# Kernel tuning notes

Hardware: AMD Instinct MI355X
Metric: run time of the kernel (lower is better)

Reference implementation:

```python
import jax, jax.numpy as jnp
import numpy as np

B, S, D, H = 2, 2048, 1024, 16
HD = D // H


def setup_inputs() -> dict:
    key = jax.random.key(0)
    ks = jax.random.split(key, 9)
    std = 0.02
    return {
        "x": jax.random.normal(ks[0], (B, S, D), dtype=jnp.float32),
        "wq": jax.random.normal(ks[1], (D, D), dtype=jnp.float32) * std,
        "bq": jnp.zeros((D,), dtype=jnp.float32),
        "wk": jax.random.normal(ks[2], (D, D), dtype=jnp.float32) * std,
        "bk": jnp.zeros((D,), dtype=jnp.float32),
        "wv": jax.random.normal(ks[3], (D, D), dtype=jnp.float32) * std,
        "bv": jnp.zeros((D,), dtype=jnp.float32),
        "wo": jax.random.normal(ks[4], (D, D), dtype=jnp.float32) * std,
        "bo": jnp.zeros((D,), dtype=jnp.float32),
    }


def reference(x, wq, bq, wk, bk, wv, bv, wo, bo):
    bsz, seq_len, d_model = x.shape
    # projections: torch Linear computes x @ W.T + b with W of shape (out, in)
    q = (x @ wq.T + bq).reshape(bsz, seq_len, H, HD).transpose(0, 2, 1, 3)  # bhsd
    k = (x @ wk.T + bk).reshape(bsz, seq_len, H, HD).transpose(0, 2, 1, 3)
    v = (x @ wv.T + bv).reshape(bsz, seq_len, H, HD).transpose(0, 2, 1, 3)
    scale = HD ** -0.5
    scores = jnp.einsum("bhqd,bhkd->bhqk", q, k) * scale  # [B,H,S,S]
    causal = jnp.tril(jnp.ones((seq_len, seq_len), dtype=bool))
    scores = jnp.where(causal[None, None], scores, -jnp.inf)
    attn = jax.nn.softmax(scores, axis=-1)
    ctx = jnp.einsum("bhqk,bhkd->bhqd", attn, v)
    ctx = ctx.transpose(0, 2, 1, 3).reshape(bsz, seq_len, d_model)
    return ctx @ wo.T + bo
```

## Files before the change

### kernel.cpp

```cpp
#include <hip/hip_runtime.h>
#include <hip/hip_bf16.h>

#define B_  2
#define S_  2048
#define D_  1024
#define H_  16
#define HD_ 64
#define M_  (B_ * S_)

typedef __bf16 bf16;
typedef __bf16 bf16x4 __attribute__((ext_vector_type(4)));
typedef __bf16 bf16x8 __attribute__((ext_vector_type(8)));
typedef float  f32x4  __attribute__((ext_vector_type(4)));

__device__ __forceinline__ bf16x8 ld8g(const bf16* p) { return *(const bf16x8*)p; }

#define GLL(g, l) __builtin_amdgcn_global_load_lds( \
    (const __attribute__((address_space(1))) void*)(g), \
    (__attribute__((address_space(3))) void*)(l), 16, 0, 0)

__global__ __launch_bounds__(256) void convert_kernel(
    const float* __restrict__ x,  const float* __restrict__ wq,
    const float* __restrict__ wk, const float* __restrict__ wv,
    const float* __restrict__ wo,
    bf16* __restrict__ xb,  bf16* __restrict__ wqb, bf16* __restrict__ wkb,
    bf16* __restrict__ wvb, bf16* __restrict__ wob)
{
    const int seg = blockIdx.y;
    const float* src;
    bf16* dst;
    if (seg < 4)      { src = x  + (long)seg * 1048576; dst = xb  + (long)seg * 1048576; }
    else if (seg == 4){ src = wq; dst = wqb; }
    else if (seg == 5){ src = wk; dst = wkb; }
    else if (seg == 6){ src = wv; dst = wvb; }
    else              { src = wo; dst = wob; }
    const long i = ((long)blockIdx.x * 256 + threadIdx.x) * 8;
    float4 a = *(const float4*)(src + i);
    float4 b = *(const float4*)(src + i + 4);
    bf16x8 r;
    r[0] = (bf16)a.x; r[1] = (bf16)a.y; r[2] = (bf16)a.z; r[3] = (bf16)a.w;
    r[4] = (bf16)b.x; r[5] = (bf16)b.y; r[6] = (bf16)b.z; r[7] = (bf16)b.w;
    *(bf16x8*)(dst + i) = r;
}

__device__ __forceinline__ void gemm_acc_bk32(
    const bf16* __restrict__ A, const bf16* __restrict__ Bt,
    f32x4 (&acc)[4][4])
{
    __shared__ bf16 As[128 * 32];
    __shared__ bf16 Bs[128 * 32];

    const int tid  = threadIdx.x;
    const int wave = tid >> 6;
    const int lane = tid & 63;
    const int quad = lane >> 4;
    const int l15  = lane & 15;
    const int wr   = (wave >> 1) * 64;
    const int wc   = (wave & 1) * 64;
    const int m0   = blockIdx.y * 128;
    const int n0   = blockIdx.x * 128;

    const int sr = wave * 16 + (lane >> 2);
    const int sc = (lane & 3) * 8;
    const bf16* Ag = A  + (long)(m0 + sr) * D_ + sc;
    const bf16* Bg = Bt + (long)(n0 + sr) * D_ + sc;
    bf16* lA = As + wave * 512;
    bf16* lB = Bs + wave * 512;

    for (int k0 = 0; k0 < D_; k0 += 32) {
        __syncthreads();
        GLL(Ag + k0,             lA);
        GLL(Ag + 64 * D_ + k0,   lA + 64 * 32);
        GLL(Bg + k0,             lB);
        GLL(Bg + 64 * D_ + k0,   lB + 64 * 32);
        __syncthreads();

        bf16x8 af[4], bfr[4];
        for (int mi = 0; mi < 4; mi++)
            af[mi] = *(const bf16x8*)&As[(wr + mi * 16 + l15) * 32 + quad * 8];
        for (int ni = 0; ni < 4; ni++)
            bfr[ni] = *(const bf16x8*)&Bs[(wc + ni * 16 + l15) * 32 + quad * 8];

        for (int mi = 0; mi < 4; mi++)
            for (int ni = 0; ni < 4; ni++)
                acc[mi][ni] = __builtin_amdgcn_mfma_f32_16x16x32_bf16(
                    af[mi], bfr[ni], acc[mi][ni], 0, 0, 0);
    }
}

__global__ __launch_bounds__(256) void gemm_qkv(
    const bf16* __restrict__ xb,
    const bf16* __restrict__ wqb, const bf16* __restrict__ wkb, const bf16* __restrict__ wvb,
    const float* __restrict__ bq, const float* __restrict__ bk, const float* __restrict__ bv,
    bf16* __restrict__ qb, bf16* __restrict__ kb, bf16* __restrict__ vt)
{
    const bf16*  Bt   = (blockIdx.z == 0) ? wqb : (blockIdx.z == 1) ? wkb : wvb;
    const float* bias = (blockIdx.z == 0) ? bq  : (blockIdx.z == 1) ? bk  : bv;

    f32x4 acc[4][4] = {};
    gemm_acc_bk32(xb, Bt, acc);

    const int lane = threadIdx.x & 63;
    const int wave = threadIdx.x >> 6;
    const int quad = lane >> 4;
    const int l15  = lane & 15;
    const int wr   = (wave >> 1) * 64;
    const int wc   = (wave & 1) * 64;
    const int m0   = blockIdx.y * 128;
    const int n0   = blockIdx.x * 128;

    if (blockIdx.z < 2) {
        bf16* Cout = (blockIdx.z == 0) ? qb : kb;
        for (int ni = 0; ni < 4; ni++) {
            const int col = n0 + wc + ni * 16 + l15;
            const float bv = bias[col];
            for (int mi = 0; mi < 4; mi++) {
                const int rowb = m0 + wr + mi * 16 + quad * 4;
                for (int r = 0; r < 4; r++)
                    Cout[(long)(rowb + r) * D_ + col] = (bf16)(acc[mi][ni][r] + bv);
            }
        }
    } else {
        for (int ni = 0; ni < 4; ni++) {
            const int col = n0 + wc + ni * 16 + l15;
            const float bv = bias[col];
            const int h = col >> 6, hd = col & (HD_ - 1);
            for (int mi = 0; mi < 4; mi++) {
                const int rowb = m0 + wr + mi * 16 + quad * 4;
                const int b = rowb >> 11;
                const int s0 = rowb & (S_ - 1);
                bf16x4 v4;
                for (int r = 0; r < 4; r++) v4[r] = (bf16)(acc[mi][ni][r] + bv);
                *(bf16x4*)&vt[(((long)(b * H_ + h)) * HD_ + hd) * S_ + s0] = v4;
            }
        }
    }
}

__global__ __launch_bounds__(256) void gemm_out(
    const bf16* __restrict__ cb, const bf16* __restrict__ wob,
    const float* __restrict__ bo, float* __restrict__ out)
{
    f32x4 acc[4][4] = {};
    gemm_acc_bk32(cb, wob, acc);

    const int lane = threadIdx.x & 63;
    const int wave = threadIdx.x >> 6;
    const int quad = lane >> 4;
    const int l15  = lane & 15;
    const int wr   = (wave >> 1) * 64;
    const int wc   = (wave & 1) * 64;
    const int m0   = blockIdx.y * 128;
    const int n0   = blockIdx.x * 128;

    for (int ni = 0; ni < 4; ni++) {
        const int col = n0 + wc + ni * 16 + l15;
        const float bv = bo[col];
        for (int mi = 0; mi < 4; mi++) {
            const int rowb = m0 + wr + mi * 16 + quad * 4;
            for (int r = 0; r < 4; r++)
                out[(long)(rowb + r) * D_ + col] = acc[mi][ni][r] + bv;
        }
    }
}

__global__ __launch_bounds__(512) void attn_kernel(
    const bf16* __restrict__ Q, const bf16* __restrict__ K,
    const bf16* __restrict__ vt, bf16* __restrict__ ctx)
{
    constexpr int LDK = 72;
    __shared__ bf16 Ks[2][64 * LDK];
    __shared__ bf16 Vt[2][64 * LDK];
    __shared__ bf16 Pq[8][16 * LDK];

    const int tid  = threadIdx.x;
    const int wave = tid >> 6;
    const int lane = tid & 63;
    const int quad = lane >> 4;
    const int l15  = lane & 15;
    const int bh   = blockIdx.y;
    const int qt   = (blockIdx.y < 16) ? blockIdx.x : (15 - (int)blockIdx.x);
    const int b    = bh >> 4, h = bh & 15;
    const long base  = ((long)b * S_) * D_ + h * HD_;
    const bf16* Vth  = vt + (long)bh * HD_ * S_;

    const int krow = tid >> 3;
    const int kcol = (tid & 7) * 8;

    const int qw    = qt * 128 + wave * 16;
    const int qrow  = qw + l15;
    const bf16* Qr = Q + base + (long)qrow * D_;
    bf16x8 qf0 = ld8g(&Qr[quad * 8]);
    bf16x8 qf1 = ld8g(&Qr[quad * 8 + 32]);

    float l_i = 0.f;
    f32x4 o_acc[4] = {};

    auto process_tile = [&](int kbase, int buf) {
        if (kbase > qw + 15) return;
        f32x4 sc[4];
        for (int kt = 0; kt < 4; kt++) {
            const bf16* Kr = &Ks[buf][(kt * 16 + l15) * LDK + quad * 8];
            bf16x8 a0 = *(const bf16x8*)Kr;
            bf16x8 a1 = *(const bf16x8*)(Kr + 32);
            f32x4 z = {};
            z = __builtin_amdgcn_mfma_f32_16x16x32_bf16(a0, qf0, z, 0, 0, 0);
            z = __builtin_amdgcn_mfma_f32_16x16x32_bf16(a1, qf1, z, 0, 0, 0);
            sc[kt] = z;
        }
        float sum = 0.f;
        if (kbase + 63 > qw) {
            for (int kt = 0; kt < 4; kt++)
                for (int r = 0; r < 4; r++) {
                    const int k_g = kbase + kt * 16 + quad * 4 + r;
                    const float p = (k_g <= qrow) ? __expf(sc[kt][r] * 0.125f) : 0.f;
                    sc[kt][r] = p;
                    sum += p;
                }
        } else {
            for (int kt = 0; kt < 4; kt++)
                for (int r = 0; r < 4; r++) {
                    const float p = __expf(sc[kt][r] * 0.125f);
                    sc[kt][r] = p;
                    sum += p;
                }
        }
        sum += __shfl_xor(sum, 16, 64);
        sum += __shfl_xor(sum, 32, 64);
        l_i += sum;

        bf16* Pw = &Pq[wave][0];
        for (int kt = 0; kt < 4; kt++) {
            union { uint2 u; bf16 hh[4]; } pk;
            pk.hh[0] = (bf16)sc[kt][0];
            pk.hh[1] = (bf16)sc[kt][1];
            pk.hh[2] = (bf16)sc[kt][2];
            pk.hh[3] = (bf16)sc[kt][3];
            *(uint2*)&Pw[l15 * LDK + kt * 16 + quad * 4] = pk.u;
        }
        __asm__ volatile("s_waitcnt lgkmcnt(0)" ::: "memory");
        bf16x8 pf0 = *(const bf16x8*)&Pw[l15 * LDK + quad * 8];
        bf16x8 pf1 = *(const bf16x8*)&Pw[l15 * LDK + quad * 8 + 32];

        for (int ni = 0; ni < 4; ni++) {
            const bf16* Vr = &Vt[buf][(ni * 16 + l15) * LDK + quad * 8];
            bf16x8 av0 = *(const bf16x8*)Vr;
            bf16x8 av1 = *(const bf16x8*)(Vr + 32);
            o_acc[ni] = __builtin_amdgcn_mfma_f32_16x16x32_bf16(av0, pf0, o_acc[ni], 0, 0, 0);
            o_acc[ni] = __builtin_amdgcn_mfma_f32_16x16x32_bf16(av1, pf1, o_acc[ni], 0, 0, 0);
        }
    };

    bf16x8 kA = ld8g(K + base + (long)krow * D_ + kcol);
    bf16x8 wA = ld8g(Vth + (long)krow * S_ + kcol);
    bf16x8 kB = ld8g(K + base + (long)(64 + krow) * D_ + kcol);
    bf16x8 wB = ld8g(Vth + (long)krow * S_ + 64 + kcol);

    const int njt = 2 * qt + 2;
    for (int j = 0; j < njt; j += 2) {
        __syncthreads();
        *(bf16x8*)&Ks[0][krow * LDK + kcol] = kA;
        *(bf16x8*)&Vt[0][krow * LDK + kcol] = wA;
        *(bf16x8*)&Ks[1][krow * LDK + kcol] = kB;
        *(bf16x8*)&Vt[1][krow * LDK + kcol] = wB;
        if (j + 2 < njt) {
            kA = ld8g(K + base + (long)((j + 2) * 64 + krow) * D_ + kcol);
            wA = ld8g(Vth + (long)krow * S_ + (j + 2) * 64 + kcol);
            kB = ld8g(K + base + (long)((j + 3) * 64 + krow) * D_ + kcol);
            wB = ld8g(Vth + (long)krow * S_ + (j + 3) * 64 + kcol);
        }
        __syncthreads();
        process_tile(j * 64, 0);
        process_tile(j * 64 + 64, 1);
    }

    const float invl = 1.f / l_i;
    bf16* Pw = &Pq[wave][0];
    for (int ni = 0; ni < 4; ni++)
        for (int r = 0; r < 4; r++)
            Pw[l15 * LDK + ni * 16 + quad * 4 + r] = (bf16)(o_acc[ni][r] * invl);
    __asm__ volatile("s_waitcnt lgkmcnt(0)" ::: "memory");
    for (int round = 0; round < 2; round++) {
        const int rowq = (lane >> 3) + round * 8;
        bf16x8 val = *(const bf16x8*)&Pw[rowq * LDK + (lane & 7) * 8];
        const int q_g = qt * 128 + wave * 16 + rowq;
        *(bf16x8*)&ctx[base + (long)q_g * D_ + (lane & 7) * 8] = val;
    }
}

extern "C" void kernel_launch(void* const* d_in, const int* in_sizes, int n_in,
                              void* d_out, int out_size, void* d_ws, size_t ws_size,
                              hipStream_t stream)
{
    const float* x  = (const float*)d_in[0];
    const float* wq = (const float*)d_in[1];
    const float* bq = (const float*)d_in[2];
    const float* wk = (const float*)d_in[3];
    const float* bk = (const float*)d_in[4];
    const float* wv = (const float*)d_in[5];
    const float* bv = (const float*)d_in[6];
    const float* wo = (const float*)d_in[7];
    const float* bo = (const float*)d_in[8];
    float* out = (float*)d_out;

    const long NX = (long)M_ * D_;
    const long NW = (long)D_ * D_;
    bf16* xb  = (bf16*)d_ws;
    bf16* wqb = xb  + NX;
    bf16* wkb = wqb + NW;
    bf16* wvb = wkb + NW;
    bf16* wob = wvb + NW;
    bf16* qb  = wob + NW;
    bf16* kb  = qb  + NX;
    bf16* vt  = kb  + NX;
    bf16* cb  = xb;

    dim3 blk(256, 1, 1);

    convert_kernel<<<dim3(512, 8), blk, 0, stream>>>(
        x, wq, wk, wv, wo, xb, wqb, wkb, wvb, wob);

    gemm_qkv<<<dim3(8, 32, 3), blk, 0, stream>>>(
        xb, wqb, wkb, wvb, bq, bk, bv, qb, kb, vt);

    attn_kernel<<<dim3(16, 32), dim3(512, 1, 1), 0, stream>>>(qb, kb, vt, cb);

    gemm_out<<<dim3(8, 32), blk, 0, stream>>>(cb, wob, bo, out);
}
```

Measured before the change: 182.7 us.

## Remap block indices for XCD locality and shrink output GEMM tiles

```diff
diff --git a/kernel.cpp b/kernel.cpp
--- a/kernel.cpp
+++ b/kernel.cpp
@@ -45,7 +45,7 @@
 
 __device__ __forceinline__ void gemm_acc_bk32(
     const bf16* __restrict__ A, const bf16* __restrict__ Bt,
-    f32x4 (&acc)[4][4])
+    f32x4 (&acc)[4][4], int m0, int n0)
 {
     __shared__ bf16 As[128 * 32];
     __shared__ bf16 Bs[128 * 32];
@@ -57,8 +57,6 @@
     const int l15  = lane & 15;
     const int wr   = (wave >> 1) * 64;
     const int wc   = (wave & 1) * 64;
-    const int m0   = blockIdx.y * 128;
-    const int n0   = blockIdx.x * 128;
 
     const int sr = wave * 16 + (lane >> 2);
     const int sc = (lane & 3) * 8;
@@ -94,11 +92,18 @@
     const float* __restrict__ bq, const float* __restrict__ bk, const float* __restrict__ bv,
     bf16* __restrict__ qb, bf16* __restrict__ kb, bf16* __restrict__ vt)
 {
-    const bf16*  Bt   = (blockIdx.z == 0) ? wqb : (blockIdx.z == 1) ? wkb : wvb;
-    const float* bias = (blockIdx.z == 0) ? bq  : (blockIdx.z == 1) ? bk  : bv;
+    const int bid = blockIdx.x;
+    const int z   = bid >> 8;
+    const int r   = bid & 255;
+    const int Y   = (r & 7) * 4 + ((r >> 3) & 3);
+    const int X   = r >> 5;
+    const int m0  = Y * 128, n0 = X * 128;
+
+    const bf16*  Bt   = (z == 0) ? wqb : (z == 1) ? wkb : wvb;
+    const float* bias = (z == 0) ? bq  : (z == 1) ? bk  : bv;
 
     f32x4 acc[4][4] = {};
-    gemm_acc_bk32(xb, Bt, acc);
+    gemm_acc_bk32(xb, Bt, acc, m0, n0);
 
     const int lane = threadIdx.x & 63;
     const int wave = threadIdx.x >> 6;
@@ -106,18 +111,16 @@
     const int l15  = lane & 15;
     const int wr   = (wave >> 1) * 64;
     const int wc   = (wave & 1) * 64;
-    const int m0   = blockIdx.y * 128;
-    const int n0   = blockIdx.x * 128;
-
-    if (blockIdx.z < 2) {
-        bf16* Cout = (blockIdx.z == 0) ? qb : kb;
+
+    if (z < 2) {
+        bf16* Cout = (z == 0) ? qb : kb;
         for (int ni = 0; ni < 4; ni++) {
             const int col = n0 + wc + ni * 16 + l15;
             const float bv = bias[col];
             for (int mi = 0; mi < 4; mi++) {
                 const int rowb = m0 + wr + mi * 16 + quad * 4;
-                for (int r = 0; r < 4; r++)
-                    Cout[(long)(rowb + r) * D_ + col] = (bf16)(acc[mi][ni][r] + bv);
+                for (int r2 = 0; r2 < 4; r2++)
+                    Cout[(long)(rowb + r2) * D_ + col] = (bf16)(acc[mi][ni][r2] + bv);
             }
         }
     } else {
@@ -130,7 +133,7 @@
                 const int b = rowb >> 11;
                 const int s0 = rowb & (S_ - 1);
                 bf16x4 v4;
-                for (int r = 0; r < 4; r++) v4[r] = (bf16)(acc[mi][ni][r] + bv);
+                for (int r2 = 0; r2 < 4; r2++) v4[r2] = (bf16)(acc[mi][ni][r2] + bv);
                 *(bf16x4*)&vt[(((long)(b * H_ + h)) * HD_ + hd) * S_ + s0] = v4;
             }
         }
@@ -141,45 +144,78 @@
     const bf16* __restrict__ cb, const bf16* __restrict__ wob,
     const float* __restrict__ bo, float* __restrict__ out)
 {
-    f32x4 acc[4][4] = {};
-    gemm_acc_bk32(cb, wob, acc);
-
-    const int lane = threadIdx.x & 63;
-    const int wave = threadIdx.x >> 6;
-    const int quad = lane >> 4;
-    const int l15  = lane & 15;
-    const int wr   = (wave >> 1) * 64;
-    const int wc   = (wave & 1) * 64;
-    const int m0   = blockIdx.y * 128;
-    const int n0   = blockIdx.x * 128;
-
-    for (int ni = 0; ni < 4; ni++) {
-        const int col = n0 + wc + ni * 16 + l15;
-        const float bv = bo[col];
-        for (int mi = 0; mi < 4; mi++) {
-            const int rowb = m0 + wr + mi * 16 + quad * 4;
-            for (int r = 0; r < 4; r++)
-                out[(long)(rowb + r) * D_ + col] = acc[mi][ni][r] + bv;
-        }
-    }
-}
-
-__global__ __launch_bounds__(512) void attn_kernel(
-    const bf16* __restrict__ Q, const bf16* __restrict__ K,
-    const bf16* __restrict__ vt, bf16* __restrict__ ctx)
-{
-    constexpr int LDK = 72;
-    __shared__ bf16 Ks[2][64 * LDK];
-    __shared__ bf16 Vt[2][64 * LDK];
-    __shared__ bf16 Pq[8][16 * LDK];
+    __shared__ bf16 As[128 * 32];
+    __shared__ bf16 Bs[64 * 32];
+
+    const int bid = blockIdx.x;
+    const int Y   = (bid & 7) * 4 + ((bid >> 3) & 3);
+    const int X   = bid >> 5;
+    const int m0  = Y * 128, n0 = X * 64;
 
     const int tid  = threadIdx.x;
     const int wave = tid >> 6;
     const int lane = tid & 63;
     const int quad = lane >> 4;
     const int l15  = lane & 15;
-    const int bh   = blockIdx.y;
-    const int qt   = (blockIdx.y < 16) ? blockIdx.x : (15 - (int)blockIdx.x);
+    const int wr   = (wave >> 1) * 64;
+    const int wc   = (wave & 1) * 32;
+
+    const int sr = wave * 16 + (lane >> 2);
+    const int sc = (lane & 3) * 8;
+    const bf16* Ag = cb  + (long)(m0 + sr) * D_ + sc;
+    const bf16* Bg = wob + (long)(n0 + sr) * D_ + sc;
+    bf16* lA = As + wave * 512;
+    bf16* lB = Bs + wave * 512;
+
+    f32x4 acc[4][2] = {};
+
+    for (int k0 = 0; k0 < D_; k0 += 32) {
+        __syncthreads();
+        GLL(Ag + k0,             lA);
+        GLL(Ag + 64 * D_ + k0,   lA + 64 * 32);
+        GLL(Bg + k0,             lB);
+        __syncthreads();
+
+        bf16x8 af[4], bfr[2];
+        for (int mi = 0; mi < 4; mi++)
+            af[mi] = *(const bf16x8*)&As[(wr + mi * 16 + l15) * 32 + quad * 8];
+        for (int ni = 0; ni < 2; ni++)
+            bfr[ni] = *(const bf16x8*)&Bs[(wc + ni * 16 + l15) * 32 + quad * 8];
+
+        for (int mi = 0; mi < 4; mi++)
+            for (int ni = 0; ni < 2; ni++)
+                acc[mi][ni] = __builtin_amdgcn_mfma_f32_16x16x32_bf16(
+                    af[mi], bfr[ni], acc[mi][ni], 0, 0, 0);
+    }
+
+    for (int ni = 0; ni < 2; ni++) {
+        const int col = n0 + wc + ni * 16 + l15;
+        const float bv = bo[col];
+        for (int mi = 0; mi < 4; mi++) {
+            const int rowb = m0 + wr + mi * 16 + quad * 4;
+            for (int r2 = 0; r2 < 4; r2++)
+                out[(long)(rowb + r2) * D_ + col] = acc[mi][ni][r2] + bv;
+        }
+    }
+}
+
+__global__ __launch_bounds__(512) void attn_kernel(
+    const bf16* __restrict__ Q, const bf16* __restrict__ K,
+    const bf16* __restrict__ vt, bf16* __restrict__ ctx)
+{
+    constexpr int LDK = 72;
+    __shared__ bf16 Ks[2][64 * LDK];
+    __shared__ bf16 Vt[2][64 * LDK];
+    __shared__ bf16 Pq[8][16 * LDK];
+
+    const int tid  = threadIdx.x;
+    const int wave = tid >> 6;
+    const int lane = tid & 63;
+    const int quad = lane >> 4;
+    const int l15  = lane & 15;
+    const int bh   = blockIdx.x;
+    const int qy   = blockIdx.y;
+    const int qt   = (qy < 8) ? qy : (23 - qy);
     const int b    = bh >> 4, h = bh & 15;
     const long base  = ((long)b * S_) * D_ + h * HD_;
     const bf16* Vth  = vt + (long)bh * HD_ * S_;
@@ -320,10 +356,10 @@
     convert_kernel<<<dim3(512, 8), blk, 0, stream>>>(
         x, wq, wk, wv, wo, xb, wqb, wkb, wvb, wob);
 
-    gemm_qkv<<<dim3(8, 32, 3), blk, 0, stream>>>(
+    gemm_qkv<<<dim3(768, 1, 1), blk, 0, stream>>>(
         xb, wqb, wkb, wvb, bq, bk, bv, qb, kb, vt);
 
-    attn_kernel<<<dim3(16, 32), dim3(512, 1, 1), 0, stream>>>(qb, kb, vt, cb);
-
-    gemm_out<<<dim3(8, 32), blk, 0, stream>>>(cb, wob, bo, out);
-}
+    attn_kernel<<<dim3(32, 16), dim3(512, 1, 1), 0, stream>>>(qb, kb, vt, cb);
+
+    gemm_out<<<dim3(512, 1, 1), blk, 0, stream>>>(cb, wob, bo, out);
+}
```

Result: slower. 187.5 us (+2.6%).
